# Optimization experiments

Measured on AMD Instinct MI355X. Metric: run time of the kernel, lower is better.

The kernel has to match this reference:

```python
import jax, jax.numpy as jnp
import numpy as np

B, S, E = 4, 2048, 1024
H, DK = 16, 64

def setup_inputs() -> dict:
    key = jax.random.key(0)
    ks = jax.random.split(key, 9)
    sc = 1.0 / np.sqrt(E)
    return {
        "q": jax.random.normal(ks[0], (B, S, E), jnp.float32),
        "Wq": jax.random.normal(ks[1], (E, H * DK), jnp.float32) * sc,
        "bq": jax.random.normal(ks[2], (H * DK,), jnp.float32) * 0.01,
        "Wk": jax.random.normal(ks[3], (E, H * DK), jnp.float32) * sc,
        "bk": jax.random.normal(ks[4], (H * DK,), jnp.float32) * 0.01,
        "Wv": jax.random.normal(ks[5], (E, H * DK), jnp.float32) * sc,
        "bv": jax.random.normal(ks[6], (H * DK,), jnp.float32) * 0.01,
        "Wo": jax.random.normal(ks[7], (H * DK, E), jnp.float32) * sc,
        "bo": jax.random.normal(ks[8], (E,), jnp.float32) * 0.01,
    }

def _split_heads(x):
    # (B, S, H*DK) -> (B, H, S, DK)
    return x.reshape(B, S, H, DK).transpose(0, 2, 1, 3)

def reference(q, Wq, bq, Wk, bk, Wv, bv, Wo, bo):
    # self-attention: k = v = q (torch module path when k=v=None)
    qh = _split_heads(q @ Wq + bq)
    kh = _split_heads(q @ Wk + bk)
    vh = _split_heads(q @ Wv + bv)
    scale = 1.0 / jnp.sqrt(jnp.asarray(DK, qh.dtype))
    scores = jnp.einsum("bhqd,bhkd->bhqk", qh, kh) * scale  # (B,H,S,S)
    attn = jax.nn.softmax(scores, axis=-1)
    ctx = jnp.einsum("bhqk,bhkd->bhqd", attn, vh)
    ctx = ctx.transpose(0, 2, 1, 3).reshape(B, S, H * DK)
    return ctx @ Wo + bo
```

## Files before the change

kernel.cpp:

```cpp
#include <hip/hip_runtime.h>
#include <hip/hip_bf16.h>
#include <math.h>


typedef _Float16 f16x8 __attribute__((ext_vector_type(8)));
typedef _Float16 f16x4 __attribute__((ext_vector_type(4)));
typedef _Float16 f16x2 __attribute__((ext_vector_type(2)));
typedef float    f32x4 __attribute__((ext_vector_type(4)));
typedef unsigned int u32x2 __attribute__((ext_vector_type(2)));
typedef unsigned int u32x4 __attribute__((ext_vector_type(4)));

#define MFMA16(a,b,c) __builtin_amdgcn_mfma_f32_16x16x32_f16(a,b,c,0,0,0)

__device__ __forceinline__ void async_cp16(const _Float16* g, _Float16* l) {
    __builtin_amdgcn_global_load_lds(
        (const __attribute__((address_space(1))) unsigned int*)g,
        (__attribute__((address_space(3))) unsigned int*)l,
        16, 0, 0);
}

__device__ __forceinline__ f16x2 pk(float a, float b) {
    return __builtin_bit_cast(f16x2, __builtin_amdgcn_cvt_pkrtz(a, b));
}

__global__ void __launch_bounds__(256) prep_weights(
    const float* __restrict__ Wq, const float* __restrict__ Wk,
    const float* __restrict__ Wv, const float* __restrict__ Wo,
    _Float16* __restrict__ wt)
{
    __shared__ float tile[32][33];
    int mat = blockIdx.y;
    const float* W = (mat==0)?Wq:(mat==1)?Wk:(mat==2)?Wv:Wo;
    _Float16* WT = wt + (size_t)mat*1048576;
    int t = blockIdx.x;
    int kb = (t & 31) * 32;
    int nb = (t >> 5) * 32;
    int tx = threadIdx.x & 31, ty = threadIdx.x >> 5;
    #pragma unroll
    for (int r = 0; r < 4; ++r) {
        int row = ty + r*8;
        tile[row][tx] = W[(size_t)(kb+row)*1024 + nb + tx];
    }
    __syncthreads();
    #pragma unroll
    for (int r = 0; r < 4; ++r) {
        int row = ty + r*8;
        WT[(size_t)(nb+row)*1024 + kb + tx] = (_Float16)tile[tx][row];
    }
}

__global__ void __launch_bounds__(256) cvt_x(
    const float* __restrict__ X, _Float16* __restrict__ Xh)
{
    int i = (blockIdx.x*256 + threadIdx.x)*4;
    f32x4 x = *(const f32x4*)&X[i];
    f16x4 h;
    #pragma unroll
    for (int k=0;k<4;k++) h[k] = (_Float16)x[k];
    *(f16x4*)&Xh[i] = h;
}

__global__ void __launch_bounds__(256) gemm_qkv(
    const _Float16* __restrict__ Xh, const _Float16* __restrict__ wt,
    const float* __restrict__ bq, const float* __restrict__ bk, const float* __restrict__ bv,
    _Float16* __restrict__ Q, _Float16* __restrict__ K, _Float16* __restrict__ Vt)
{
    __shared__ __align__(16) _Float16 sA[8192];
    __shared__ __align__(16) _Float16 sB[8192];

    const int id = blockIdx.x;
    const int xcd = id & 7;
    const int lid = id >> 3;
    const int ng  = lid / 64;
    const int rem = lid % 64;
    const int mq  = rem >> 5;
    const int r2  = rem & 31;
    const int m_lo = r2 >> 3;
    const int nb   = r2 & 7;
    const int mblk = (mq*4 + m_lo)*8 + xcd;
    const int nblk = ng*8 + nb;

    const int tid = threadIdx.x;
    const int wave = tid >> 6, lane = tid & 63;
    const int wr = wave >> 1, wc = wave & 1;
    const int q4 = lane >> 4, cc = lane & 15;

    const int mat = nblk >> 3;
    const int colbase = (nblk & 7) * 128;
    const _Float16* Bg = wt + (size_t)mat*1048576 + (size_t)colbase*1024;
    const _Float16* Ag = Xh + (size_t)mblk*131072;

    f32x4 acc[4][4] = {};

    const int srow = tid >> 3;
    const int scg  = ((tid & 7) ^ ((tid >> 3) & 7)) * 8;

    for (int kb = 0; kb < 1024; kb += 64) {
        __syncthreads();
        #pragma unroll
        for (int rr = 0; rr < 4; ++rr) {
            async_cp16(&Ag[(size_t)(rr*32 + srow)*1024 + kb + scg], sA + rr*2048 + wave*512);
            async_cp16(&Bg[(size_t)(rr*32 + srow)*1024 + kb + scg], sB + rr*2048 + wave*512);
        }
        __syncthreads();
        #pragma unroll
        for (int ks = 0; ks < 2; ++ks) {
            f16x8 af[4], bf[4];
            #pragma unroll
            for (int i=0;i<4;i++){
                af[i] = *(const f16x8*)&sA[(wr*64+i*16+cc)*64 + ((ks*4+q4)^(cc&7))*8];
                bf[i] = *(const f16x8*)&sB[(wc*64+i*16+cc)*64 + ((ks*4+q4)^(cc&7))*8];
            }
            #pragma unroll
            for (int i=0;i<4;i++)
                #pragma unroll
                for (int j=0;j<4;j++)
                    acc[i][j] = MFMA16(af[i], bf[j], acc[i][j]);
        }
    }

    const float* bias = (mat==0)?bq:(mat==1)?bk:bv;
    const float QSCALE = 0.125f * 1.44269504f;
    #pragma unroll
    for (int i=0;i<4;i++)
      #pragma unroll
      for (int j=0;j<4;j++)
        #pragma unroll
        for (int r=0;r<4;r++){
            int m = mblk*128 + wr*64 + i*16 + q4*4 + r;
            int ncol = colbase + wc*64 + j*16 + cc;
            float val = acc[i][j][r] + bias[ncol];
            int b = m >> 11, s = m & 2047;
            int h = ncol >> 6, dk = ncol & 63;
            if (mat == 2) {
                Vt[((size_t)(b*16+h)*64 + dk)*2048 + s] = (_Float16)val;
            } else {
                size_t qi = ((size_t)(b*16+h)*2048 + s)*64 + dk;
                if (mat == 0) Q[qi] = (_Float16)(val * QSCALE);
                else          K[qi] = (_Float16)val;
            }
        }
}

__global__ void __launch_bounds__(256) gemm_out(
    const _Float16* __restrict__ Ctx, const _Float16* __restrict__ wt,
    const float* __restrict__ bo,
    float* __restrict__ out)
{
    __shared__ __align__(16) _Float16 sA[8192];
    __shared__ __align__(16) _Float16 sB[8192];

    const int id = blockIdx.x;
    const int xcd = id & 7;
    const int lid = id >> 3;
    const int mq  = lid >> 5;
    const int r2  = lid & 31;
    const int m_lo = r2 >> 3;
    const int nblk = r2 & 7;
    const int mblk = (mq*4 + m_lo)*8 + xcd;

    const int tid = threadIdx.x;
    const int wave = tid >> 6, lane = tid & 63;
    const int wr = wave >> 1, wc = wave & 1;
    const int q4 = lane >> 4, cc = lane & 15;

    const _Float16* Bg = wt + (size_t)3*1048576 + (size_t)nblk*128*1024;
    const _Float16* Ag = Ctx + (size_t)mblk*131072;

    f32x4 acc[4][4] = {};
    const int srow = tid >> 3;
    const int scg  = ((tid & 7) ^ ((tid >> 3) & 7)) * 8;

    for (int kb = 0; kb < 1024; kb += 64) {
        __syncthreads();
        #pragma unroll
        for (int rr = 0; rr < 4; ++rr) {
            async_cp16(&Ag[(size_t)(rr*32 + srow)*1024 + kb + scg], sA + rr*2048 + wave*512);
            async_cp16(&Bg[(size_t)(rr*32 + srow)*1024 + kb + scg], sB + rr*2048 + wave*512);
        }
        __syncthreads();
        #pragma unroll
        for (int ks = 0; ks < 2; ++ks) {
            f16x8 af[4], bf[4];
            #pragma unroll
            for (int i=0;i<4;i++){
                af[i] = *(const f16x8*)&sA[(wr*64+i*16+cc)*64 + ((ks*4+q4)^(cc&7))*8];
                bf[i] = *(const f16x8*)&sB[(wc*64+i*16+cc)*64 + ((ks*4+q4)^(cc&7))*8];
            }
            #pragma unroll
            for (int i=0;i<4;i++)
                #pragma unroll
                for (int j=0;j<4;j++)
                    acc[i][j] = MFMA16(af[i], bf[j], acc[i][j]);
        }
    }

    #pragma unroll
    for (int i=0;i<4;i++)
      #pragma unroll
      for (int j=0;j<4;j++)
        #pragma unroll
        for (int r=0;r<4;r++){
            int m = mblk*128 + wr*64 + i*16 + q4*4 + r;
            int n = nblk*128 + wc*64 + j*16 + cc;
            out[(size_t)m*1024 + n] = acc[i][j][r] + bo[n];
        }
}

__global__ void __launch_bounds__(256,3) attn(
    const _Float16* __restrict__ Qg, const _Float16* __restrict__ Kg,
    const _Float16* __restrict__ Vg,
    _Float16* __restrict__ Ctx)
{
    __shared__ __align__(16) _Float16 sK[128][72];
    __shared__ __align__(16) _Float16 sV[64][136];

    const int id = blockIdx.x;
    const int xcd = id & 7;
    const int t2 = id >> 3;
    const int qc = t2 & 15;
    const int bh = (t2 >> 4) * 8 + xcd;

    const int tid = threadIdx.x;
    const int wave = tid >> 6, lane = tid & 63;
    const int q4 = lane >> 4, cc = lane & 15;

    const size_t hoff = (size_t)bh * 131072;
    const _Float16* Qp = Qg + hoff;
    const _Float16* Kp = Kg + hoff;
    const _Float16* Vp = Vg + hoff;

    const int qbase = qc*128 + wave*32;

    f16x8 qf[2][2];
    #pragma unroll
    for (int m=0;m<2;m++)
      #pragma unroll
      for (int ks=0;ks<2;ks++)
        qf[m][ks] = *(const f16x8*)&Qp[(qbase+m*16+cc)*64 + ks*32 + q4*8];

    f32x4 o[2][4] = {};
    float lsum[2] = {0.f, 0.f};

    const int r0 = tid >> 3, c8 = (tid & 7)*8;
    const int vrow = tid >> 4, vg = (tid & 15)*8;

    f16x8 kr[4], vr[4];
    #pragma unroll
    for (int p=0;p<4;p++){
        kr[p] = *(const f16x8*)&Kp[(p*32 + r0)*64 + c8];
        vr[p] = *(const f16x8*)&Vp[(size_t)(p*16 + vrow)*2048 + vg];
    }

    for (int kt = 0; kt < 16; ++kt) {
        __syncthreads();
        #pragma unroll
        for (int p=0;p<4;p++){
            *(f16x8*)&sK[p*32+r0][c8] = kr[p];
            *(f16x8*)&sV[p*16+vrow][vg] = vr[p];
        }
        __syncthreads();
        if (kt < 15) {
            #pragma unroll
            for (int p=0;p<4;p++){
                kr[p] = *(const f16x8*)&Kp[((kt+1)*128 + p*32 + r0)*64 + c8];
                vr[p] = *(const f16x8*)&Vp[(size_t)(p*16 + vrow)*2048 + (kt+1)*128 + vg];
            }
        }

        #pragma unroll
        for (int ks=0;ks<4;ks++){
            unsigned Ud[2][2], Wd[2][2];
            #pragma unroll
            for (int aa=0;aa<2;aa++){
                int kj = ks*2 + aa;
                f16x8 k0 = *(const f16x8*)&sK[kj*16+cc][q4*8];
                f16x8 k1 = *(const f16x8*)&sK[kj*16+cc][32+q4*8];
                #pragma unroll
                for (int m=0;m<2;m++){
                    f32x4 z = {};
                    f32x4 s = MFMA16(k0, qf[m][0], z);
                    s = MFMA16(k1, qf[m][1], s);
                    float p0 = __builtin_amdgcn_exp2f(s[0]);
                    float p1 = __builtin_amdgcn_exp2f(s[1]);
                    float p2 = __builtin_amdgcn_exp2f(s[2]);
                    float p3 = __builtin_amdgcn_exp2f(s[3]);
                    lsum[m] += (p0 + p1) + (p2 + p3);
                    unsigned d0 = __builtin_bit_cast(unsigned, pk(p0, p1));
                    unsigned d1 = __builtin_bit_cast(unsigned, pk(p2, p3));
                    if (aa == 0) { Ud[m][0] = d0; Ud[m][1] = d1; }
                    else         { Wd[m][0] = d0; Wd[m][1] = d1; }
                }
            }
            f16x8 pa[2];
            #pragma unroll
            for (int m=0;m<2;m++){
                u32x2 x0 = __builtin_amdgcn_permlane32_swap(Ud[m][0], Wd[m][0], false, false);
                u32x2 r02 = __builtin_amdgcn_permlane16_swap(x0[0], x0[1], false, false);
                u32x2 x1 = __builtin_amdgcn_permlane32_swap(Ud[m][1], Wd[m][1], false, false);
                u32x2 r13 = __builtin_amdgcn_permlane16_swap(x1[0], x1[1], false, false);
                u32x4 pw;
                pw[0] = r02[0]; pw[1] = r13[0]; pw[2] = r02[1]; pw[3] = r13[1];
                pa[m] = __builtin_bit_cast(f16x8, pw);
            }
            #pragma unroll
            for (int v=0;v<4;v++){
                f16x8 vf = *(const f16x8*)&sV[v*16+cc][ks*32+q4*8];
                o[0][v] = MFMA16(pa[0], vf, o[0][v]);
                o[1][v] = MFMA16(pa[1], vf, o[1][v]);
            }
        }
    }

    #pragma unroll
    for (int m=0;m<2;m++){
        lsum[m] += __shfl_xor(lsum[m], 16, 64);
        lsum[m] += __shfl_xor(lsum[m], 32, 64);
    }
    __syncthreads();
    float* sL = (float*)&sK[0][0];
    if (q4 == 0) {
        sL[wave*32 + cc]      = lsum[0];
        sL[wave*32 + 16 + cc] = lsum[1];
    }
    __syncthreads();

    int b = bh >> 4, h = bh & 15;
    #pragma unroll
    for (int m=0;m<2;m++)
      #pragma unroll
      for (int r=0;r<4;r++){
        float inv = 1.f / sL[wave*32 + m*16 + q4*4 + r];
        int s = qbase + m*16 + q4*4 + r;
        #pragma unroll
        for (int v=0;v<4;v++){
            float val = o[m][v][r]*inv;
            int dk = v*16 + cc;
            Ctx[((size_t)(b*2048+s)*16 + h)*64 + dk] = (_Float16)val;
        }
      }
}

extern "C" void kernel_launch(void* const* d_in, const int* in_sizes, int n_in,
                              void* d_out, int out_size, void* d_ws, size_t ws_size,
                              hipStream_t stream)
{
    const float* q  = (const float*)d_in[0];
    const float* Wq = (const float*)d_in[1];
    const float* bq = (const float*)d_in[2];
    const float* Wk = (const float*)d_in[3];
    const float* bk = (const float*)d_in[4];
    const float* Wv = (const float*)d_in[5];
    const float* bv = (const float*)d_in[6];
    const float* Wo = (const float*)d_in[7];
    const float* bo = (const float*)d_in[8];
    float* out = (float*)d_out;

    _Float16* ws  = (_Float16*)d_ws;
    _Float16* wt  = ws;
    _Float16* Xh  = ws + 4194304;
    _Float16* Q   = ws + 12582912;
    _Float16* K   = ws + 20971520;
    _Float16* Vt  = ws + 29360128;
    _Float16* Ctx = Xh;

    prep_weights<<<dim3(1024,4), 256, 0, stream>>>(Wq, Wk, Wv, Wo, wt);
    cvt_x<<<dim3(8192), 256, 0, stream>>>(q, Xh);
    gemm_qkv<<<dim3(1536), 256, 0, stream>>>(Xh, wt, bq, bk, bv, Q, K, Vt);
    attn<<<dim3(1024), 256, 0, stream>>>(Q, K, Vt, Ctx);
    gemm_out<<<dim3(512), 256, 0, stream>>>(Ctx, wt, bo, out);
}
```

Before: 297.7 us.

## Load K/V tiles via async global-to-LDS copies with XOR-swizzled layout

The register-staged K/V prefetch with padded LDS arrays is replaced by direct global_load_lds copies into unpadded, XOR-swizzled LDS tiles, and the LDS fragment reads are updated to match the swizzle. This frees the prefetch registers and lets the launch bound rise from 3 to 4 blocks per CU. The loads are no longer overlapped with compute, because each iteration waits for vmcnt(0) before the barrier, so memory latency is exposed unless the extra occupancy hides it.

```diff
diff --git a/kernel.cpp b/kernel.cpp
--- a/kernel.cpp
+++ b/kernel.cpp
@@ -207,13 +207,14 @@
         }
 }
 
-__global__ void __launch_bounds__(256,3) attn(
+__global__ void __launch_bounds__(256,4) attn(
     const _Float16* __restrict__ Qg, const _Float16* __restrict__ Kg,
     const _Float16* __restrict__ Vg,
     _Float16* __restrict__ Ctx)
 {
-    __shared__ __align__(16) _Float16 sK[128][72];
-    __shared__ __align__(16) _Float16 sV[64][136];
+    __shared__ __align__(16) _Float16 sK[8192];
+    __shared__ __align__(16) _Float16 sV[8192];
+    __shared__ float sL[128];
 
     const int id = blockIdx.x;
     const int xcd = id & 7;
@@ -242,31 +243,22 @@
     f32x4 o[2][4] = {};
     float lsum[2] = {0.f, 0.f};
 
-    const int r0 = tid >> 3, c8 = (tid & 7)*8;
-    const int vrow = tid >> 4, vg = (tid & 15)*8;
-
-    f16x8 kr[4], vr[4];
-    #pragma unroll
-    for (int p=0;p<4;p++){
-        kr[p] = *(const f16x8*)&Kp[(p*32 + r0)*64 + c8];
-        vr[p] = *(const f16x8*)&Vp[(size_t)(p*16 + vrow)*2048 + vg];
-    }
+    const int srow = tid >> 3;
+    const int scg  = ((tid & 7) ^ ((tid >> 3) & 7)) * 8;
+    const int vrow = tid >> 4;
+    const int vsg  = ((tid & 15) ^ ((tid >> 4) & 7)) * 8;
 
     for (int kt = 0; kt < 16; ++kt) {
         __syncthreads();
-        #pragma unroll
-        for (int p=0;p<4;p++){
-            *(f16x8*)&sK[p*32+r0][c8] = kr[p];
-            *(f16x8*)&sV[p*16+vrow][vg] = vr[p];
-        }
-        __syncthreads();
-        if (kt < 15) {
-            #pragma unroll
-            for (int p=0;p<4;p++){
-                kr[p] = *(const f16x8*)&Kp[((kt+1)*128 + p*32 + r0)*64 + c8];
-                vr[p] = *(const f16x8*)&Vp[(size_t)(p*16 + vrow)*2048 + (kt+1)*128 + vg];
-            }
-        }
+        const _Float16* Kb = Kp + kt*8192;
+        const _Float16* Vb = Vp + (size_t)kt*128;
+        #pragma unroll
+        for (int rr = 0; rr < 4; ++rr) {
+            async_cp16(&Kb[(rr*32 + srow)*64 + scg],          sK + rr*2048 + wave*512);
+            async_cp16(&Vb[(size_t)(rr*16 + vrow)*2048 + vsg], sV + rr*2048 + wave*512);
+        }
+        asm volatile("s_waitcnt vmcnt(0)" ::: "memory");
+        __syncthreads();
 
         #pragma unroll
         for (int ks=0;ks<4;ks++){
@@ -274,8 +266,8 @@
             #pragma unroll
             for (int aa=0;aa<2;aa++){
                 int kj = ks*2 + aa;
-                f16x8 k0 = *(const f16x8*)&sK[kj*16+cc][q4*8];
-                f16x8 k1 = *(const f16x8*)&sK[kj*16+cc][32+q4*8];
+                f16x8 k0 = *(const f16x8*)&sK[(kj*16+cc)*64 + ((q4    ^(cc&7))*8)];
+                f16x8 k1 = *(const f16x8*)&sK[(kj*16+cc)*64 + (((4+q4)^(cc&7))*8)];
                 #pragma unroll
                 for (int m=0;m<2;m++){
                     f32x4 z = {};
@@ -305,7 +297,7 @@
             }
             #pragma unroll
             for (int v=0;v<4;v++){
-                f16x8 vf = *(const f16x8*)&sV[v*16+cc][ks*32+q4*8];
+                f16x8 vf = *(const f16x8*)&sV[(v*16+cc)*128 + (((ks*4+q4)^(cc&7))*8)];
                 o[0][v] = MFMA16(pa[0], vf, o[0][v]);
                 o[1][v] = MFMA16(pa[1], vf, o[1][v]);
             }
@@ -317,8 +309,6 @@
         lsum[m] += __shfl_xor(lsum[m], 16, 64);
         lsum[m] += __shfl_xor(lsum[m], 32, 64);
     }
-    __syncthreads();
-    float* sL = (float*)&sK[0][0];
     if (q4 == 0) {
         sL[wave*32 + cc]      = lsum[0];
         sL[wave*32 + 16 + cc] = lsum[1];
```

New measurement: 313.7 us. 1.05x slower.
